# Kernel tuning notes

Measured on AMD Instinct MI355X. Metric: run time of the kernel, lower is better.

Reference implementation:

```python
import jax, jax.numpy as jnp
import numpy as np

D = 131072   # input_dim = 2*256*256
H = 512      # lstm_hidden_dim
OUT = 128    # out_dim


def _lstm_cell(x, h, c, W_ih, W_hh, b_ih, b_hh):
    # PyTorch LSTMCell: gates in order (i, f, g, o)
    gates = x @ W_ih.T + b_ih + h @ W_hh.T + b_hh  # [1, 4H]
    i, f, g, o = jnp.split(gates, 4, axis=-1)
    i = jax.nn.sigmoid(i)
    f = jax.nn.sigmoid(f)
    g = jnp.tanh(g)
    o = jax.nn.sigmoid(o)
    c_new = f * c + i * g
    h_new = o * jnp.tanh(c_new)
    return h_new, c_new


def setup_inputs() -> dict:
    key = jax.random.key(0)
    ks = jax.random.split(key, 20)
    s_ih = 1.0 / np.sqrt(H)
    inp = {
        "dL_dU": jax.random.normal(ks[0], (256, 256), jnp.float32),
        "dL_dV": jax.random.normal(ks[1], (256, 256), jnp.float32),
        "hidden": jax.random.normal(ks[2], (2, 1, H), jnp.float32),
        "cell": jax.random.normal(ks[3], (2, 1, H), jnp.float32),
        "W_ih1": jax.random.uniform(ks[4], (4 * H, D), jnp.float32, -s_ih, s_ih),
        "W_hh1": jax.random.uniform(ks[5], (4 * H, H), jnp.float32, -s_ih, s_ih),
        "b_ih1": jax.random.uniform(ks[6], (4 * H,), jnp.float32, -s_ih, s_ih),
        "b_hh1": jax.random.uniform(ks[7], (4 * H,), jnp.float32, -s_ih, s_ih),
        "W_ih2": jax.random.uniform(ks[8], (4 * H, H), jnp.float32, -s_ih, s_ih),
        "W_hh2": jax.random.uniform(ks[9], (4 * H, H), jnp.float32, -s_ih, s_ih),
        "b_ih2": jax.random.uniform(ks[10], (4 * H,), jnp.float32, -s_ih, s_ih),
        "b_hh2": jax.random.uniform(ks[11], (4 * H,), jnp.float32, -s_ih, s_ih),
        "W1": jax.random.uniform(ks[12], (OUT * OUT, H), jnp.float32, -s_ih, s_ih),
        "b1": jax.random.uniform(ks[13], (OUT * OUT,), jnp.float32, -s_ih, s_ih),
        "W2": jax.random.uniform(ks[14], (1, H), jnp.float32, -s_ih, s_ih),
        "b2": jax.random.uniform(ks[15], (1,), jnp.float32, -s_ih, s_ih),
        "W3": jax.random.uniform(ks[16], (1, H), jnp.float32, -s_ih, s_ih),
        "b3": jax.random.uniform(ks[17], (1,), jnp.float32, -s_ih, s_ih),
    }
    return inp


def reference(dL_dU, dL_dV, hidden, cell,
              W_ih1, W_hh1, b_ih1, b_hh1,
              W_ih2, W_hh2, b_ih2, b_hh2,
              W1, b1, W2, b2, W3, b3):
    grad_flat = jnp.concatenate([dL_dU.reshape(-1), dL_dV.reshape(-1)], axis=0)[None, :]  # [1, D]
    h0, c0 = _lstm_cell(grad_flat, hidden[0], cell[0], W_ih1, W_hh1, b_ih1, b_hh1)
    h1, c1 = _lstm_cell(h0, hidden[1], cell[1], W_ih2, W_hh2, b_ih2, b_hh2)
    g = (h1 @ W1.T + b1).reshape(OUT, OUT)
    step_size = jnp.clip(h1 @ W2.T + b2, 1e-07, 0.005)
    m_c = jnp.clip(2.0 * jnp.clip(h0 @ W3.T + b3, 0.0, 1.0), 0.0, 1.0)
    return (g, step_size, m_c, jnp.stack((h0, h1)), jnp.stack((c0, c1)))
```

## Files before the change

### kernel.cpp

```cpp
#include <hip/hip_runtime.h>
#include <math.h>

#define D_IN 131072
#define H 512
#define G4 2048
#define OUTN 16384

#define OFF_STEP 16384
#define OFF_MC   16385
#define OFF_H0   16386
#define OFF_H1   16898
#define OFF_C0   17410
#define OFF_C1   17922

__device__ __forceinline__ float sigmoidf_(float x) {
    return 1.0f / (1.0f + __expf(-x));
}

__device__ __forceinline__ float dot4(float4 a, float4 b) {
    return a.x*b.x + a.y*b.y + a.z*b.z + a.w*b.w;
}

__global__ __launch_bounds__(256) void k_gemv1(
    const float* __restrict__ U, const float* __restrict__ V,
    const float* __restrict__ Wih, const float* __restrict__ Whh,
    const float* __restrict__ bih, const float* __restrict__ bhh,
    const float* __restrict__ hidden, float* __restrict__ gates)
{
    const int r = blockIdx.x;
    const int t = threadIdx.x;
    const float4* __restrict__ Wrow = (const float4*)(Wih + (size_t)r * D_IN);
    const float4* __restrict__ U4 = (const float4*)U;
    const float4* __restrict__ V4 = (const float4*)V;
    float acc = 0.0f;
    #pragma unroll 4
    for (int idx = t; idx < 32768; idx += 256) {
        float4 w = Wrow[idx];
        float4 x = (idx < 16384) ? U4[idx] : V4[idx - 16384];
        acc += dot4(w, x);
    }
    if (t < 128) {
        const float4* Wh4 = (const float4*)(Whh + (size_t)r * H);
        const float4* h4  = (const float4*)hidden;
        acc += dot4(Wh4[t], h4[t]);
    }
    #pragma unroll
    for (int off = 32; off > 0; off >>= 1) acc += __shfl_down(acc, off);
    __shared__ float s[4];
    if ((t & 63) == 0) s[t >> 6] = acc;
    __syncthreads();
    if (t == 0) {
        gates[r] = s[0] + s[1] + s[2] + s[3] + bih[r] + bhh[r];
    }
}

__global__ __launch_bounds__(512) void k_cell1(
    const float* __restrict__ gates, const float* __restrict__ cell_in,
    const float* __restrict__ W3, const float* __restrict__ b3,
    float* __restrict__ h0, float* __restrict__ c0, float* __restrict__ out)
{
    const int j = threadIdx.x;
    float ig = sigmoidf_(gates[j]);
    float fg = sigmoidf_(gates[H + j]);
    float gg = tanhf(gates[2*H + j]);
    float og = sigmoidf_(gates[3*H + j]);
    float c  = fg * cell_in[j] + ig * gg;
    float h  = og * tanhf(c);
    h0[j] = h;  c0[j] = c;
    out[OFF_H0 + j] = h;
    out[OFF_C0 + j] = c;
    float p = h * W3[j];
    #pragma unroll
    for (int off = 32; off > 0; off >>= 1) p += __shfl_down(p, off);
    __shared__ float s[8];
    if ((j & 63) == 0) s[j >> 6] = p;
    __syncthreads();
    if (j == 0) {
        float v = s[0]+s[1]+s[2]+s[3]+s[4]+s[5]+s[6]+s[7] + b3[0];
        v = fminf(fmaxf(v, 0.0f), 1.0f);
        v = fminf(2.0f * v, 1.0f);
        out[OFF_MC] = v;
    }
}

__global__ __launch_bounds__(256) void k_gemv2(
    const float* __restrict__ Wih, const float* __restrict__ Whh,
    const float* __restrict__ bih, const float* __restrict__ bhh,
    const float* __restrict__ h0, const float* __restrict__ hidden,
    float* __restrict__ gates2)
{
    const int wave = (blockIdx.x * 256 + threadIdx.x) >> 6;
    const int lane = threadIdx.x & 63;
    if (wave >= G4) return;
    const float4* Wr = (const float4*)(Wih + (size_t)wave * H);
    const float4* Hr = (const float4*)(Whh + (size_t)wave * H);
    const float4* x4 = (const float4*)h0;
    const float4* y4 = (const float4*)(hidden + H);
    float acc = 0.0f;
    #pragma unroll
    for (int k = lane; k < 128; k += 64) {
        acc += dot4(Wr[k], x4[k]);
        acc += dot4(Hr[k], y4[k]);
    }
    #pragma unroll
    for (int off = 32; off > 0; off >>= 1) acc += __shfl_down(acc, off);
    if (lane == 0) gates2[wave] = acc + bih[wave] + bhh[wave];
}

__global__ __launch_bounds__(512) void k_cell2(
    const float* __restrict__ gates2, const float* __restrict__ cell_in,
    const float* __restrict__ W2, const float* __restrict__ b2,
    float* __restrict__ h1, float* __restrict__ c1, float* __restrict__ out)
{
    const int j = threadIdx.x;
    float ig = sigmoidf_(gates2[j]);
    float fg = sigmoidf_(gates2[H + j]);
    float gg = tanhf(gates2[2*H + j]);
    float og = sigmoidf_(gates2[3*H + j]);
    float c  = fg * cell_in[H + j] + ig * gg;
    float h  = og * tanhf(c);
    h1[j] = h;  c1[j] = c;
    out[OFF_H1 + j] = h;
    out[OFF_C1 + j] = c;
    float p = h * W2[j];
    #pragma unroll
    for (int off = 32; off > 0; off >>= 1) p += __shfl_down(p, off);
    __shared__ float s[8];
    if ((j & 63) == 0) s[j >> 6] = p;
    __syncthreads();
    if (j == 0) {
        float v = s[0]+s[1]+s[2]+s[3]+s[4]+s[5]+s[6]+s[7] + b2[0];
        v = fminf(fmaxf(v, 1e-7f), 0.005f);
        out[OFF_STEP] = v;
    }
}

__global__ __launch_bounds__(256) void k_out_g(
    const float* __restrict__ W1, const float* __restrict__ b1,
    const float* __restrict__ h1, float* __restrict__ out)
{
    const int wave = (blockIdx.x * 256 + threadIdx.x) >> 6;
    const int lane = threadIdx.x & 63;
    if (wave >= OUTN) return;
    const float4* Wr = (const float4*)(W1 + (size_t)wave * H);
    const float4* x4 = (const float4*)h1;
    float acc = 0.0f;
    #pragma unroll
    for (int k = lane; k < 128; k += 64) {
        acc += dot4(Wr[k], x4[k]);
    }
    #pragma unroll
    for (int off = 32; off > 0; off >>= 1) acc += __shfl_down(acc, off);
    if (lane == 0) out[wave] = acc + b1[wave];
}

extern "C" void kernel_launch(void* const* d_in, const int* in_sizes, int n_in,
                              void* d_out, int out_size, void* d_ws, size_t ws_size,
                              hipStream_t stream) {
    const float* dL_dU  = (const float*)d_in[0];
    const float* dL_dV  = (const float*)d_in[1];
    const float* hidden = (const float*)d_in[2];
    const float* cell   = (const float*)d_in[3];
    const float* W_ih1  = (const float*)d_in[4];
    const float* W_hh1  = (const float*)d_in[5];
    const float* b_ih1  = (const float*)d_in[6];
    const float* b_hh1  = (const float*)d_in[7];
    const float* W_ih2  = (const float*)d_in[8];
    const float* W_hh2  = (const float*)d_in[9];
    const float* b_ih2  = (const float*)d_in[10];
    const float* b_hh2  = (const float*)d_in[11];
    const float* W1     = (const float*)d_in[12];
    const float* b1     = (const float*)d_in[13];
    const float* W2     = (const float*)d_in[14];
    const float* b2     = (const float*)d_in[15];
    const float* W3     = (const float*)d_in[16];
    const float* b3     = (const float*)d_in[17];

    float* out = (float*)d_out;
    float* ws  = (float*)d_ws;
    float* gates1 = ws;
    float* h0     = ws + 2048;
    float* c0     = ws + 2560;
    float* gates2 = ws + 3072;
    float* h1     = ws + 5120;
    float* c1     = ws + 5632;

    k_gemv1<<<G4, 256, 0, stream>>>(dL_dU, dL_dV, W_ih1, W_hh1, b_ih1, b_hh1,
                                    hidden, gates1);
    k_cell1<<<1, 512, 0, stream>>>(gates1, cell, W3, b3, h0, c0, out);
    k_gemv2<<<G4/4, 256, 0, stream>>>(W_ih2, W_hh2, b_ih2, b_hh2, h0, hidden, gates2);
    k_cell2<<<1, 512, 0, stream>>>(gates2, cell, W2, b2, h1, c1, out);
    k_out_g<<<OUTN/4, 256, 0, stream>>>(W1, b1, h1, out);
    (void)in_sizes; (void)n_in; (void)out_size; (void)ws_size;
}
```

Before: 208.6 us.

## Fuse LSTM cell activations into downstream GEMV kernels, splitting gemv1 loop

Folds each single-block LSTM cell kernel into the following GEMV kernel. Every block recomputes the 512 cell activations into shared memory, and block 0 writes the h/c outputs and the scalar heads. This cuts the launch count from five to three and removes the global round trips for h0 and h1. The cost is redundant activation math in every block (128 and 1024 blocks). Separately, the first GEMV loop is split into two loops over U and V to drop the per-iteration branch.

Result: no change. 206.9 us (-0.8%).

```diff
diff --git a/kernel.cpp b/kernel.cpp
--- a/kernel.cpp
+++ b/kernel.cpp
@@ -34,10 +34,12 @@
     const float4* __restrict__ V4 = (const float4*)V;
     float acc = 0.0f;
     #pragma unroll 4
-    for (int idx = t; idx < 32768; idx += 256) {
-        float4 w = Wrow[idx];
-        float4 x = (idx < 16384) ? U4[idx] : V4[idx - 16384];
-        acc += dot4(w, x);
+    for (int idx = t; idx < 16384; idx += 256) {
+        acc += dot4(Wrow[idx], U4[idx]);
+    }
+    #pragma unroll 4
+    for (int idx = t; idx < 16384; idx += 256) {
+        acc += dot4(Wrow[idx + 16384], V4[idx]);
     }
     if (t < 128) {
         const float4* Wh4 = (const float4*)(Whh + (size_t)r * H);
@@ -54,104 +56,104 @@
     }
 }
 
-__global__ __launch_bounds__(512) void k_cell1(
-    const float* __restrict__ gates, const float* __restrict__ cell_in,
+__global__ __launch_bounds__(1024) void k_l2fused(
+    const float* __restrict__ gates1, const float* __restrict__ cell_in,
+    const float* __restrict__ hidden,
+    const float* __restrict__ Wih2, const float* __restrict__ Whh2,
+    const float* __restrict__ bih2, const float* __restrict__ bhh2,
     const float* __restrict__ W3, const float* __restrict__ b3,
-    float* __restrict__ h0, float* __restrict__ c0, float* __restrict__ out)
+    float* __restrict__ gates2, float* __restrict__ out)
 {
-    const int j = threadIdx.x;
-    float ig = sigmoidf_(gates[j]);
-    float fg = sigmoidf_(gates[H + j]);
-    float gg = tanhf(gates[2*H + j]);
-    float og = sigmoidf_(gates[3*H + j]);
-    float c  = fg * cell_in[j] + ig * gg;
-    float h  = og * tanhf(c);
-    h0[j] = h;  c0[j] = c;
-    out[OFF_H0 + j] = h;
-    out[OFF_C0 + j] = c;
-    float p = h * W3[j];
+    __shared__ float h0s[H];
+    __shared__ float red[16];
+    const int tid = threadIdx.x;
+    if (tid < H) {
+        float ig = sigmoidf_(gates1[tid]);
+        float fg = sigmoidf_(gates1[H + tid]);
+        float gg = tanhf(gates1[2*H + tid]);
+        float og = sigmoidf_(gates1[3*H + tid]);
+        float c  = fg * cell_in[tid] + ig * gg;
+        float h  = og * tanhf(c);
+        h0s[tid] = h;
+        if (blockIdx.x == 0) {
+            out[OFF_H0 + tid] = h;
+            out[OFF_C0 + tid] = c;
+        }
+    }
+    __syncthreads();
+    const int wv = tid >> 6, lane = tid & 63;
+    const int row = blockIdx.x * 16 + wv;
+    const float4* __restrict__ Wr = (const float4*)(Wih2 + (size_t)row * H);
+    const float4* __restrict__ Hr = (const float4*)(Whh2 + (size_t)row * H);
+    const float4* h4 = (const float4*)h0s;
+    const float4* __restrict__ y4 = (const float4*)(hidden + H);
+    float acc = dot4(Wr[lane],      h4[lane])      + dot4(Hr[lane],      y4[lane])
+              + dot4(Wr[lane + 64], h4[lane + 64]) + dot4(Hr[lane + 64], y4[lane + 64]);
     #pragma unroll
-    for (int off = 32; off > 0; off >>= 1) p += __shfl_down(p, off);
-    __shared__ float s[8];
-    if ((j & 63) == 0) s[j >> 6] = p;
-    __syncthreads();
-    if (j == 0) {
-        float v = s[0]+s[1]+s[2]+s[3]+s[4]+s[5]+s[6]+s[7] + b3[0];
-        v = fminf(fmaxf(v, 0.0f), 1.0f);
-        v = fminf(2.0f * v, 1.0f);
-        out[OFF_MC] = v;
+    for (int off = 32; off > 0; off >>= 1) acc += __shfl_down(acc, off);
+    if (lane == 0) gates2[row] = acc + bih2[row] + bhh2[row];
+
+    if (blockIdx.x == 0) {
+        float p = (tid < H) ? h0s[tid] * W3[tid] : 0.0f;
+        #pragma unroll
+        for (int off = 32; off > 0; off >>= 1) p += __shfl_down(p, off);
+        if (lane == 0) red[wv] = p;
+        __syncthreads();
+        if (tid == 0) {
+            float v = b3[0];
+            #pragma unroll
+            for (int i = 0; i < 16; ++i) v += red[i];
+            v = fminf(fmaxf(v, 0.0f), 1.0f);
+            out[OFF_MC] = fminf(2.0f * v, 1.0f);
+        }
     }
 }
 
-__global__ __launch_bounds__(256) void k_gemv2(
-    const float* __restrict__ Wih, const float* __restrict__ Whh,
-    const float* __restrict__ bih, const float* __restrict__ bhh,
-    const float* __restrict__ h0, const float* __restrict__ hidden,
-    float* __restrict__ gates2)
+__global__ __launch_bounds__(1024) void k_l3fused(
+    const float* __restrict__ gates2, const float* __restrict__ cell_in,
+    const float* __restrict__ W1, const float* __restrict__ b1,
+    const float* __restrict__ W2, const float* __restrict__ b2,
+    float* __restrict__ out)
 {
-    const int wave = (blockIdx.x * 256 + threadIdx.x) >> 6;
-    const int lane = threadIdx.x & 63;
-    if (wave >= G4) return;
-    const float4* Wr = (const float4*)(Wih + (size_t)wave * H);
-    const float4* Hr = (const float4*)(Whh + (size_t)wave * H);
-    const float4* x4 = (const float4*)h0;
-    const float4* y4 = (const float4*)(hidden + H);
-    float acc = 0.0f;
-    #pragma unroll
-    for (int k = lane; k < 128; k += 64) {
-        acc += dot4(Wr[k], x4[k]);
-        acc += dot4(Hr[k], y4[k]);
+    __shared__ float h1s[H];
+    __shared__ float red[16];
+    const int tid = threadIdx.x;
+    if (tid < H) {
+        float ig = sigmoidf_(gates2[tid]);
+        float fg = sigmoidf_(gates2[H + tid]);
+        float gg = tanhf(gates2[2*H + tid]);
+        float og = sigmoidf_(gates2[3*H + tid]);
+        float c  = fg * cell_in[H + tid] + ig * gg;
+        float h  = og * tanhf(c);
+        h1s[tid] = h;
+        if (blockIdx.x == 0) {
+            out[OFF_H1 + tid] = h;
+            out[OFF_C1 + tid] = c;
+        }
     }
+    __syncthreads();
+    const int wv = tid >> 6, lane = tid & 63;
+    const int row = blockIdx.x * 16 + wv;
+    const float4* __restrict__ Wr = (const float4*)(W1 + (size_t)row * H);
+    const float4* h4 = (const float4*)h1s;
+    float acc = dot4(Wr[lane], h4[lane]) + dot4(Wr[lane + 64], h4[lane + 64]);
     #pragma unroll
     for (int off = 32; off > 0; off >>= 1) acc += __shfl_down(acc, off);
-    if (lane == 0) gates2[wave] = acc + bih[wave] + bhh[wave];
-}
+    if (lane == 0) out[row] = acc + b1[row];
 
-__global__ __launch_bounds__(512) void k_cell2(
-    const float* __restrict__ gates2, const float* __restrict__ cell_in,
-    const float* __restrict__ W2, const float* __restrict__ b2,
-    float* __restrict__ h1, float* __restrict__ c1, float* __restrict__ out)
-{
-    const int j = threadIdx.x;
-    float ig = sigmoidf_(gates2[j]);
-    float fg = sigmoidf_(gates2[H + j]);
-    float gg = tanhf(gates2[2*H + j]);
-    float og = sigmoidf_(gates2[3*H + j]);
-    float c  = fg * cell_in[H + j] + ig * gg;
-    float h  = og * tanhf(c);
-    h1[j] = h;  c1[j] = c;
-    out[OFF_H1 + j] = h;
-    out[OFF_C1 + j] = c;
-    float p = h * W2[j];
-    #pragma unroll
-    for (int off = 32; off > 0; off >>= 1) p += __shfl_down(p, off);
-    __shared__ float s[8];
-    if ((j & 63) == 0) s[j >> 6] = p;
-    __syncthreads();
-    if (j == 0) {
-        float v = s[0]+s[1]+s[2]+s[3]+s[4]+s[5]+s[6]+s[7] + b2[0];
-        v = fminf(fmaxf(v, 1e-7f), 0.005f);
-        out[OFF_STEP] = v;
+    if (blockIdx.x == 0) {
+        float p = (tid < H) ? h1s[tid] * W2[tid] : 0.0f;
+        #pragma unroll
+        for (int off = 32; off > 0; off >>= 1) p += __shfl_down(p, off);
+        if (lane == 0) red[wv] = p;
+        __syncthreads();
+        if (tid == 0) {
+            float v = b2[0];
+            #pragma unroll
+            for (int i = 0; i < 16; ++i) v += red[i];
+            out[OFF_STEP] = fminf(fmaxf(v, 1e-7f), 0.005f);
+        }
     }
-}
-
-__global__ __launch_bounds__(256) void k_out_g(
-    const float* __restrict__ W1, const float* __restrict__ b1,
-    const float* __restrict__ h1, float* __restrict__ out)
-{
-    const int wave = (blockIdx.x * 256 + threadIdx.x) >> 6;
-    const int lane = threadIdx.x & 63;
-    if (wave >= OUTN) return;
-    const float4* Wr = (const float4*)(W1 + (size_t)wave * H);
-    const float4* x4 = (const float4*)h1;
-    float acc = 0.0f;
-    #pragma unroll
-    for (int k = lane; k < 128; k += 64) {
-        acc += dot4(Wr[k], x4[k]);
-    }
-    #pragma unroll
-    for (int off = 32; off > 0; off >>= 1) acc += __shfl_down(acc, off);
-    if (lane == 0) out[wave] = acc + b1[wave];
 }
 
 extern "C" void kernel_launch(void* const* d_in, const int* in_sizes, int n_in,
@@ -179,17 +181,13 @@
     float* out = (float*)d_out;
     float* ws  = (float*)d_ws;
     float* gates1 = ws;
-    float* h0     = ws + 2048;
-    float* c0     = ws + 2560;
-    float* gates2 = ws + 3072;
-    float* h1     = ws + 5120;
-    float* c1     = ws + 5632;
+    float* gates2 = ws + 2048;
 
     k_gemv1<<<G4, 256, 0, stream>>>(dL_dU, dL_dV, W_ih1, W_hh1, b_ih1, b_hh1,
                                     hidden, gates1);
-    k_cell1<<<1, 512, 0, stream>>>(gates1, cell, W3, b3, h0, c0, out);
-    k_gemv2<<<G4/4, 256, 0, stream>>>(W_ih2, W_hh2, b_ih2, b_hh2, h0, hidden, gates2);
-    k_cell2<<<1, 512, 0, stream>>>(gates2, cell, W2, b2, h1, c1, out);
-    k_out_g<<<OUTN/4, 256, 0, stream>>>(W1, b1, h1, out);
+    k_l2fused<<<G4/16, 1024, 0, stream>>>(gates1, cell, hidden,
+                                          W_ih2, W_hh2, b_ih2, b_hh2,
+                                          W3, b3, gates2, out);
+    k_l3fused<<<OUTN/16, 1024, 0, stream>>>(gates2, cell, W1, b1, W2, b2, out);
     (void)in_sizes; (void)n_in; (void)out_size; (void)ws_size;
 }
```
